# Performance work log

Measured on AMD Instinct MI355X. Metric: run time of the kernel, lower is better.

Reference implementation:

```python
import jax, jax.numpy as jnp
import numpy as np

EMBED = 1024
HEADS = 16
HEAD_DIM = EMBED // HEADS
HIDDEN = 4096
EPS = 1e-6


def _layer_norm(x, gamma, beta):
    mu = jnp.mean(x, axis=-1, keepdims=True)
    var = jnp.mean(jnp.square(x - mu), axis=-1, keepdims=True)
    return (x - mu) * jax.lax.rsqrt(var + EPS) * gamma + beta


def setup_inputs() -> dict:
    key = jax.random.key(0)
    ks = jax.random.split(key, 16)
    s = 1.0 / np.sqrt(EMBED)
    sh = 1.0 / np.sqrt(HIDDEN)
    return {
        "x": jax.random.normal(ks[0], (2, 2048, EMBED), dtype=jnp.float32),
        "Wq": jax.random.uniform(ks[1], (EMBED, EMBED), jnp.float32, -s, s),
        "bq": jnp.zeros((EMBED,), jnp.float32),
        "Wk": jax.random.uniform(ks[2], (EMBED, EMBED), jnp.float32, -s, s),
        "bk": jnp.zeros((EMBED,), jnp.float32),
        "Wv": jax.random.uniform(ks[3], (EMBED, EMBED), jnp.float32, -s, s),
        "bv": jnp.zeros((EMBED,), jnp.float32),
        "Wo": jax.random.uniform(ks[4], (EMBED, EMBED), jnp.float32, -s, s),
        "bo": jnp.zeros((EMBED,), jnp.float32),
        "ln1_g": jnp.ones((EMBED,), jnp.float32),
        "ln1_b": jnp.zeros((EMBED,), jnp.float32),
        "W1": jax.random.uniform(ks[5], (EMBED, HIDDEN), jnp.float32, -s, s),
        "b1": jnp.zeros((HIDDEN,), jnp.float32),
        "W2": jax.random.uniform(ks[6], (HIDDEN, EMBED), jnp.float32, -sh, sh),
        "b2": jnp.zeros((EMBED,), jnp.float32),
        "ln2_g": jnp.ones((EMBED,), jnp.float32),
        "ln2_b": jnp.zeros((EMBED,), jnp.float32),
    }


def reference(x, Wq, bq, Wk, bk, Wv, bv, Wo, bo, ln1_g, ln1_b, W1, b1, W2, b2, ln2_g, ln2_b):
    B, S, _ = x.shape
    # projections (weights stored as [in, out])
    q = (x @ Wq + bq).reshape(B, S, HEADS, HEAD_DIM)
    k = (x @ Wk + bk).reshape(B, S, HEADS, HEAD_DIM)
    v = (x @ Wv + bv).reshape(B, S, HEADS, HEAD_DIM)
    # scores: [B, H, S, S]
    scores = jnp.einsum('bqhd,bkhd->bhqk', q, k) / jnp.sqrt(jnp.float32(HEAD_DIM))
    attn = jax.nn.softmax(scores, axis=-1)
    ctx = jnp.einsum('bhqk,bkhd->bqhd', attn, v).reshape(B, S, EMBED)
    attn_out = ctx @ Wo + bo
    x1 = _layer_norm(x + attn_out, ln1_g, ln1_b)
    ffn = jax.nn.relu(x1 @ W1 + b1) @ W2 + b2
    return _layer_norm(x1 + ffn, ln2_g, ln2_b)
```

## Files before the change

kernel.cpp:

```cpp
#include <hip/hip_runtime.h>
#include <math.h>

#define EMBED 1024
#define HEADS 16
#define HDIM  64
#define HIDDEN 4096
#define BATCH 2
#define SEQ   2048
#define TOK   (BATCH * SEQ)

typedef _Float16 f16;
typedef f16 f16x8 __attribute__((ext_vector_type(8)));
typedef f16 f16x4 __attribute__((ext_vector_type(4)));
typedef float f32x4 __attribute__((ext_vector_type(4)));
typedef float f32x16 __attribute__((ext_vector_type(16)));

__device__ __forceinline__ void gload16(const void* g, void* s) {
  __builtin_amdgcn_global_load_lds(
      (const __attribute__((address_space(1))) unsigned int*)g,
      (__attribute__((address_space(3))) unsigned int*)s, 16, 0, 0);
}

template<int A16, int RELU, int OUT16, int QKV, int SPLITK>
__global__ __launch_bounds__(256, 3)
void gemm_f16(const void* __restrict__ Av, const f16* __restrict__ Wt,
              const float* __restrict__ bias0, const float* __restrict__ bias1,
              const float* __restrict__ bias2, void* __restrict__ Cv,
              int N, int K, int nbx) {
  __shared__ f16 As[512 * 8];
  __shared__ f16 Bs[512 * 8];
  const int tid = threadIdx.x;
  const int l = tid & 63, w = tid >> 6;
  const int g = l >> 4, ln = l & 15;
  int bid = blockIdx.x;
  int slice = 0;
  if (SPLITK > 1) { slice = bid % SPLITK; bid /= SPLITK; }
  const int ntiles = gridDim.x / SPLITK;
  const int cpx = ntiles >> 3;
  bid = (bid & 7) * cpx + (bid >> 3);
  const int m0 = (bid / nbx) << 7;
  const int n0 = (bid % nbx) << 7;
  const int wr = w >> 1, wc = w & 1;
  const int ksl = K / SPLITK;
  const int kbeg = slice * ksl, kend = kbeg + ksl;

  f32x4 acc[4][4] = {};

  for (int k0 = kbeg; k0 < kend; k0 += 32) {
    if (A16) {
      const f16* A = (const f16*)Av;
#pragma unroll
      for (int p = 0; p < 2; ++p) {
        const int u0 = p * 256 + w * 64;
        const int ks = u0 >> 7;
        const int row = ((u0 + l) & 127) ^ ks;
        gload16(A + (size_t)(m0 + row) * K + k0 + ks * 8, (void*)&As[u0 * 8]);
      }
    } else {
      const float* A = (const float*)Av;
      const int ks = tid & 3;
      const int r0 = tid >> 2;
#pragma unroll
      for (int p = 0; p < 2; ++p) {
        const int row = r0 + p * 64;
        const float* src = A + (size_t)(m0 + row) * K + k0 + ks * 8;
        float4 f0 = *(const float4*)src;
        float4 f1 = *(const float4*)(src + 4);
        f16x8 hh;
        hh[0] = (f16)f0.x; hh[1] = (f16)f0.y; hh[2] = (f16)f0.z; hh[3] = (f16)f0.w;
        hh[4] = (f16)f1.x; hh[5] = (f16)f1.y; hh[6] = (f16)f1.z; hh[7] = (f16)f1.w;
        *(f16x8*)&As[(ks * 128 + (row ^ ks)) * 8] = hh;
      }
    }
#pragma unroll
    for (int p = 0; p < 2; ++p) {
      const int u0 = p * 256 + w * 64;
      const int ks = u0 >> 7;
      const int col = ((u0 + l) & 127) ^ ks;
      gload16(Wt + (size_t)(n0 + col) * K + k0 + ks * 8, (void*)&Bs[u0 * 8]);
    }
    __syncthreads();
    f16x8 af[4], bf[4];
#pragma unroll
    for (int m = 0; m < 4; ++m)
      af[m] = *(const f16x8*)&As[(g * 128 + ((wr * 64 + m * 16 + ln) ^ g)) * 8];
#pragma unroll
    for (int n = 0; n < 4; ++n)
      bf[n] = *(const f16x8*)&Bs[(g * 128 + ((wc * 64 + n * 16 + ln) ^ g)) * 8];
#pragma unroll
    for (int m = 0; m < 4; ++m)
#pragma unroll
      for (int n = 0; n < 4; ++n)
        acc[m][n] = __builtin_amdgcn_mfma_f32_16x16x32_f16(af[m], bf[n], acc[m][n], 0, 0, 0);
    __syncthreads();
  }

  if (SPLITK > 1) {
    float* P = (float*)Cv + (size_t)slice * TOK * N;
#pragma unroll
    for (int m = 0; m < 4; ++m)
#pragma unroll
      for (int n = 0; n < 4; ++n)
#pragma unroll
        for (int r = 0; r < 4; ++r) {
          const size_t idx = (size_t)(m0 + wr * 64 + m * 16 + g * 4 + r) * N
                           + n0 + wc * 64 + n * 16 + ln;
          P[idx] = acc[m][n][r];
        }
    return;
  }

  const float* bp = bias0;
  int nbase = n0;
  float scale = 1.f;
  if (QKV) {
    const int seg = n0 >> 10;
    bp = (seg == 0) ? bias0 : (seg == 1) ? bias1 : bias2;
    nbase = n0 & 1023;
    if (seg == 0) scale = 0.125f * 1.44269504f;
  }
  float bv[4];
#pragma unroll
  for (int n = 0; n < 4; ++n) bv[n] = bp[nbase + wc * 64 + n * 16 + ln];
#pragma unroll
  for (int m = 0; m < 4; ++m)
#pragma unroll
    for (int n = 0; n < 4; ++n)
#pragma unroll
      for (int r = 0; r < 4; ++r) {
        float v = (acc[m][n][r] + bv[n]) * scale;
        if (RELU) v = fmaxf(v, 0.f);
        const size_t idx = (size_t)(m0 + wr * 64 + m * 16 + g * 4 + r) * N
                         + n0 + wc * 64 + n * 16 + ln;
        if (OUT16) ((f16*)Cv)[idx] = (f16)v;
        else       ((float*)Cv)[idx] = v;
      }
}

__device__ __forceinline__ unsigned kchunk(int key, int m) { return (unsigned)(m ^ (key & 7)); }

template<int BASE>
__device__ __forceinline__ f16x8 pack_frag(f32x16 p) {
  f16x8 r;
#pragma unroll
  for (int j = 0; j < 8; ++j) r[j] = (f16)p[BASE + j];
  return r;
}

#define VSTRIDE 68

__global__ __launch_bounds__(256, 2)
void attention(const f16* __restrict__ qkv, f16* __restrict__ ctx) {
  __shared__ f16 Ks[64 * 64];
  __shared__ f16 VT[64 * VSTRIDE];
  const int tid = threadIdx.x;
  const int l = tid & 63, w = tid >> 6;
  const int ln = l & 31, hi = l >> 5;
  const int bh = blockIdx.y, b = bh >> 4, h = bh & 15;
  const int q0 = blockIdx.x * 128;

  f16x8 qf[4];
  {
    const f16* qp = qkv + (size_t)(b * SEQ + q0 + w * 32 + ln) * 3072 + h * 64 + hi * 8;
#pragma unroll
    for (int kc = 0; kc < 4; ++kc) qf[kc] = *(const f16x8*)(qp + kc * 16);
  }

  f32x16 o0 = {}, o1 = {};
  float mrow = -1e30f, lrow = 0.f;

  const int skey = tid >> 3, sc = tid & 7;

  for (int kt = 0; kt < SEQ / 64; ++kt) {
    const size_t tb = (size_t)(b * SEQ + kt * 64) * 3072 + h * 64;
    f16x8 va = *(const f16x8*)(qkv + tb + 2048 + (size_t)skey * 3072 + sc * 8);
    f16x8 vb = *(const f16x8*)(qkv + tb + 2048 + (size_t)(32 + skey) * 3072 + sc * 8);
#pragma unroll
    for (int p = 0; p < 2; ++p) {
      const int key = p * 32 + skey;
      gload16(qkv + tb + 1024 + (size_t)key * 3072 + 8 * kchunk(key, sc),
              (void*)&Ks[(p * 256 + w * 64) * 8]);
    }
#pragma unroll
    for (int j = 0; j < 8; ++j) {
      const int d = sc * 8 + j;
      VT[d * VSTRIDE + skey] = va[j];
      VT[d * VSTRIDE + 32 + skey] = vb[j];
    }
    __syncthreads();

    f32x16 st0 = {}, st1 = {};
#pragma unroll
    for (int kc = 0; kc < 4; ++kc) {
      const int m = kc * 2 + hi;
      const f16x8 kf0 = *(const f16x8*)&Ks[(ln * 8 + (m ^ (ln & 7))) * 8];
      const f16x8 kf1 = *(const f16x8*)&Ks[((32 + ln) * 8 + (m ^ (ln & 7))) * 8];
      st0 = __builtin_amdgcn_mfma_f32_32x32x16_f16(kf0, qf[kc], st0, 0, 0, 0);
      st1 = __builtin_amdgcn_mfma_f32_32x32x16_f16(kf1, qf[kc], st1, 0, 0, 0);
    }

    float mt = st0[0];
#pragma unroll
    for (int r = 1; r < 16; ++r) mt = fmaxf(mt, st0[r]);
#pragma unroll
    for (int r = 0; r < 16; ++r) mt = fmaxf(mt, st1[r]);
    mt = fmaxf(mt, __shfl_xor(mt, 32));
    const float mn = fmaxf(mrow, mt);
    const float al = exp2f(mrow - mn);
    mrow = mn;
    float ps = 0.f;
#pragma unroll
    for (int r = 0; r < 16; ++r) { st0[r] = exp2f(st0[r] - mn); ps += st0[r]; }
#pragma unroll
    for (int r = 0; r < 16; ++r) { st1[r] = exp2f(st1[r] - mn); ps += st1[r]; }
    ps += __shfl_xor(ps, 32);
    lrow = lrow * al + ps;
#pragma unroll
    for (int r = 0; r < 16; ++r) { o0[r] *= al; o1[r] *= al; }

    f16x8 pf[4];
    pf[0] = pack_frag<0>(st0); pf[1] = pack_frag<8>(st0);
    pf[2] = pack_frag<0>(st1); pf[3] = pack_frag<8>(st1);

#pragma unroll
    for (int s = 0; s < 4; ++s) {
      const int k0a = 16 * s + 4 * hi;
      {
        const f16* p0 = &VT[ln * VSTRIDE + k0a];
        f16x4 x = *(const f16x4*)p0;
        f16x4 y = *(const f16x4*)(p0 + 8);
        f16x8 vf = __builtin_shufflevector(x, y, 0, 1, 2, 3, 4, 5, 6, 7);
        o0 = __builtin_amdgcn_mfma_f32_32x32x16_f16(vf, pf[s], o0, 0, 0, 0);
      }
      {
        const f16* p1 = &VT[(32 + ln) * VSTRIDE + k0a];
        f16x4 x = *(const f16x4*)p1;
        f16x4 y = *(const f16x4*)(p1 + 8);
        f16x8 vf = __builtin_shufflevector(x, y, 0, 1, 2, 3, 4, 5, 6, 7);
        o1 = __builtin_amdgcn_mfma_f32_32x32x16_f16(vf, pf[s], o1, 0, 0, 0);
      }
    }
    __syncthreads();
  }

  const float inv = 1.f / lrow;
  f16* cp = ctx + (size_t)(b * SEQ + q0 + w * 32 + ln) * EMBED + h * 64;
#pragma unroll
  for (int r = 0; r < 16; ++r) {
    const int drow = (r & 3) + 8 * (r >> 2) + 4 * hi;
    cp[drow] = (f16)(o0[r] * inv);
    cp[32 + drow] = (f16)(o1[r] * inv);
  }
}

template<int NP, int OUT16>
__global__ __launch_bounds__(256, 4)
void add_ln(const float* parts, const float* __restrict__ bias,
            const float* resid, const float* __restrict__ gam,
            const float* __restrict__ bet, float* out, f16* __restrict__ out16) {
  const int t = blockIdx.x;
  const int tid = threadIdx.x;
  const size_t base = (size_t)t * EMBED + tid * 4;
  float4 rv = *(const float4*)(resid + base);
  float4 bb = *(const float4*)(bias + tid * 4);
  float x0 = rv.x + bb.x, x1 = rv.y + bb.y, x2 = rv.z + bb.z, x3 = rv.w + bb.w;
#pragma unroll
  for (int p = 0; p < NP; ++p) {
    float4 pv = *(const float4*)(parts + (size_t)p * TOK * EMBED + base);
    x0 += pv.x; x1 += pv.y; x2 += pv.z; x3 += pv.w;
  }
  float s1 = x0 + x1 + x2 + x3;
  float s2 = x0 * x0 + x1 * x1 + x2 * x2 + x3 * x3;
  for (int off = 1; off < 64; off <<= 1) {
    s1 += __shfl_xor(s1, off);
    s2 += __shfl_xor(s2, off);
  }
  __shared__ float red[8];
  if ((tid & 63) == 0) { red[(tid >> 6) * 2] = s1; red[(tid >> 6) * 2 + 1] = s2; }
  __syncthreads();
  s1 = red[0] + red[2] + red[4] + red[6];
  s2 = red[1] + red[3] + red[5] + red[7];
  const float mu = s1 * (1.f / EMBED);
  const float var = s2 * (1.f / EMBED) - mu * mu;
  const float rstd = rsqrtf(var + 1e-6f);
  float4 gv = *(const float4*)(gam + tid * 4);
  float4 bv = *(const float4*)(bet + tid * 4);
  float4 ov;
  ov.x = (x0 - mu) * rstd * gv.x + bv.x;
  ov.y = (x1 - mu) * rstd * gv.y + bv.y;
  ov.z = (x2 - mu) * rstd * gv.z + bv.z;
  ov.w = (x3 - mu) * rstd * gv.w + bv.w;
  *(float4*)(out + base) = ov;
  if (OUT16) {
    f16x4 hh;
    hh[0] = (f16)ov.x; hh[1] = (f16)ov.y; hh[2] = (f16)ov.z; hh[3] = (f16)ov.w;
    *(f16x4*)(out16 + base) = hh;
  }
}

__device__ __forceinline__ void transpose_tile(const float* in, f16* out,
                                               int K, int N, int k0, int n0, int tid) {
  __shared__ float t[32][33];
  {
    const int ky = tid >> 3, nx = (tid & 7) * 4;
    float4 f = *(const float4*)(in + (size_t)(k0 + ky) * N + n0 + nx);
    t[ky][nx] = f.x; t[ky][nx + 1] = f.y; t[ky][nx + 2] = f.z; t[ky][nx + 3] = f.w;
  }
  __syncthreads();
  const int ny = tid >> 3, kx = (tid & 7) * 4;
  f16x4 hh;
  hh[0] = (f16)t[kx][ny];     hh[1] = (f16)t[kx + 1][ny];
  hh[2] = (f16)t[kx + 2][ny]; hh[3] = (f16)t[kx + 3][ny];
  *(f16x4*)(out + (size_t)(n0 + ny) * K + k0 + kx) = hh;
}

__global__ __launch_bounds__(256, 4)
void transpose_w(const float* __restrict__ in, f16* __restrict__ out,
                 int K, int N) {
  transpose_tile(in, out, K, N, blockIdx.y * 32, blockIdx.x * 32, threadIdx.x);
}

__global__ __launch_bounds__(256, 4)
void transpose_qkv(const float* __restrict__ w0, const float* __restrict__ w1,
                   const float* __restrict__ w2, f16* __restrict__ out) {
  const float* in = (blockIdx.z == 0) ? w0 : (blockIdx.z == 1) ? w1 : w2;
  f16* o = out + (size_t)blockIdx.z * 1024 * 1024;
  transpose_tile(in, o, 1024, 1024, blockIdx.y * 32, blockIdx.x * 32, threadIdx.x);
}

extern "C" void kernel_launch(void* const* d_in, const int* in_sizes, int n_in,
                              void* d_out, int out_size, void* d_ws, size_t ws_size,
                              hipStream_t stream) {
  const float* x    = (const float*)d_in[0];
  const float* Wq   = (const float*)d_in[1];
  const float* bq   = (const float*)d_in[2];
  const float* Wk   = (const float*)d_in[3];
  const float* bk   = (const float*)d_in[4];
  const float* Wv   = (const float*)d_in[5];
  const float* bv   = (const float*)d_in[6];
  const float* Wo   = (const float*)d_in[7];
  const float* bo   = (const float*)d_in[8];
  const float* ln1g = (const float*)d_in[9];
  const float* ln1b = (const float*)d_in[10];
  const float* W1   = (const float*)d_in[11];
  const float* b1   = (const float*)d_in[12];
  const float* W2   = (const float*)d_in[13];
  const float* b2   = (const float*)d_in[14];
  const float* ln2g = (const float*)d_in[15];
  const float* ln2b = (const float*)d_in[16];
  float* out = (float*)d_out;

  char* ws = (char*)d_ws;
  const size_t MB = 1024 * 1024;
  f16*   WtQKV = (f16*)(ws);
  f16*   WtO   = (f16*)(ws + 6 * MB);
  f16*   Wt1   = (f16*)(ws + 8 * MB);
  f16*   Wt2   = (f16*)(ws + 16 * MB);
  f16*   qkv   = (f16*)(ws + 24 * MB);
  f16*   ctx   = (f16*)(ws + 48 * MB);
  float* parts = (float*)(ws + 56 * MB);
  f16*   x1h   = (f16*)(ws + 88 * MB);
  f16*   hid   = (f16*)(ws + 24 * MB);
  float* x1    = out;

  const dim3 blk(256);
  transpose_qkv<<<dim3(32, 32, 3), blk, 0, stream>>>(Wq, Wk, Wv, WtQKV);
  transpose_w<<<dim3(32, 32), blk, 0, stream>>>(Wo, WtO, 1024, 1024);
  transpose_w<<<dim3(128, 32), blk, 0, stream>>>(W1, Wt1, 1024, 4096);
  transpose_w<<<dim3(32, 128), blk, 0, stream>>>(W2, Wt2, 4096, 1024);

  gemm_f16<0, 0, 1, 1, 1><<<768, blk, 0, stream>>>(x, WtQKV, bq, bk, bv, qkv, 3072, 1024, 24);
  attention<<<dim3(16, 32), blk, 0, stream>>>(qkv, ctx);
  gemm_f16<1, 0, 0, 0, 2><<<512, blk, 0, stream>>>(ctx, WtO, nullptr, nullptr, nullptr, parts, 1024, 1024, 8);
  add_ln<2, 1><<<4096, blk, 0, stream>>>(parts, bo, x, ln1g, ln1b, x1, x1h);
  gemm_f16<1, 1, 1, 0, 1><<<1024, blk, 0, stream>>>(x1h, Wt1, b1, nullptr, nullptr, hid, 4096, 1024, 32);
  gemm_f16<1, 0, 0, 0, 2><<<512, blk, 0, stream>>>(hid, Wt2, nullptr, nullptr, nullptr, parts, 1024, 4096, 8);
  add_ln<2, 0><<<4096, blk, 0, stream>>>(parts, b2, x1, ln2g, ln2b, out, nullptr);
}
```

Baseline: 451.7 us.

## Double-buffer K/V tiles in attention with lazy softmax rescale and swizzled V layout

The attention kernel now double-buffers the K and V^T tiles in shared memory, prefetching the next tile while computing the current one, so each iteration needs a single barrier. It adds a lazy online-softmax rescale that skips rescaling the O accumulators unless the row max grows by more than 8 (in log2 units), and tree reductions for the max and sum. It also XOR-swizzles the V^T shared layout to reduce bank conflicts and raises wave priority around the MFMA sections. The cost is double the shared-memory footprint, which may reduce occupancy, and the lazy rescale lets exponentials exceed 1 by a bounded factor, which stresses fp16 range in P.

```diff
diff --git a/kernel.cpp b/kernel.cpp
--- a/kernel.cpp
+++ b/kernel.cpp
@@ -137,8 +137,6 @@
       }
 }
 
-__device__ __forceinline__ unsigned kchunk(int key, int m) { return (unsigned)(m ^ (key & 7)); }
-
 template<int BASE>
 __device__ __forceinline__ f16x8 pack_frag(f32x16 p) {
   f16x8 r;
@@ -148,11 +146,12 @@
 }
 
 #define VSTRIDE 68
+#define NKT (SEQ / 64)
 
 __global__ __launch_bounds__(256, 2)
 void attention(const f16* __restrict__ qkv, f16* __restrict__ ctx) {
-  __shared__ f16 Ks[64 * 64];
-  __shared__ f16 VT[64 * VSTRIDE];
+  __shared__ f16 Ks[2][64 * 64];
+  __shared__ f16 VTs[2][64 * VSTRIDE];
   const int tid = threadIdx.x;
   const int l = tid & 63, w = tid >> 6;
   const int ln = l & 31, hi = l >> 5;
@@ -170,78 +169,120 @@
   float mrow = -1e30f, lrow = 0.f;
 
   const int skey = tid >> 3, sc = tid & 7;
-
-  for (int kt = 0; kt < SEQ / 64; ++kt) {
-    const size_t tb = (size_t)(b * SEQ + kt * 64) * 3072 + h * 64;
-    f16x8 va = *(const f16x8*)(qkv + tb + 2048 + (size_t)skey * 3072 + sc * 8);
-    f16x8 vb = *(const f16x8*)(qkv + tb + 2048 + (size_t)(32 + skey) * 3072 + sc * 8);
+  const f16* kbase = qkv + (size_t)(b * SEQ) * 3072 + 1024 + h * 64;
+  const f16* vbase = qkv + (size_t)(b * SEQ) * 3072 + 2048 + h * 64;
+  const int wbase = sc * 8 * VSTRIDE + (skey ^ (sc << 2));
+
+  auto gloadK = [&](int buf, int kt) {
 #pragma unroll
     for (int p = 0; p < 2; ++p) {
       const int key = p * 32 + skey;
-      gload16(qkv + tb + 1024 + (size_t)key * 3072 + 8 * kchunk(key, sc),
-              (void*)&Ks[(p * 256 + w * 64) * 8]);
-    }
+      gload16(kbase + (size_t)(kt * 64 + key) * 3072 + 8 * (sc ^ (key & 7)),
+              (void*)&Ks[buf][(p * 256 + w * 64) * 8]);
+    }
+  };
+  auto scatterV = [&](int buf, f16x8 va, f16x8 vb2) {
 #pragma unroll
     for (int j = 0; j < 8; ++j) {
-      const int d = sc * 8 + j;
-      VT[d * VSTRIDE + skey] = va[j];
-      VT[d * VSTRIDE + 32 + skey] = vb[j];
-    }
-    __syncthreads();
-
+      VTs[buf][wbase + VSTRIDE * j] = va[j];
+      VTs[buf][wbase + VSTRIDE * j + 32] = vb2[j];
+    }
+  };
+
+  {
+    const f16* vp = vbase + (size_t)skey * 3072 + sc * 8;
+    f16x8 va = *(const f16x8*)vp;
+    f16x8 vb2 = *(const f16x8*)(vp + (size_t)32 * 3072);
+    gloadK(0, 0);
+    scatterV(0, va, vb2);
+  }
+  __syncthreads();
+
+  const int sw0 = (ln >> 3) << 2;
+  const int db0 = ln * VSTRIDE, db1 = (32 + ln) * VSTRIDE;
+
+  auto body = [&](int kt, int cur) {
+    const int nxt = cur ^ 1;
+    f16x8 vna = {}, vnb = {};
+    const bool more = (kt + 1 < NKT);
+    if (more) {
+      const f16* vp = vbase + (size_t)((kt + 1) * 64 + skey) * 3072 + sc * 8;
+      vna = *(const f16x8*)vp;
+      vnb = *(const f16x8*)(vp + (size_t)32 * 3072);
+      gloadK(nxt, kt + 1);
+    }
     f32x16 st0 = {}, st1 = {};
+    __builtin_amdgcn_s_setprio(1);
 #pragma unroll
     for (int kc = 0; kc < 4; ++kc) {
       const int m = kc * 2 + hi;
-      const f16x8 kf0 = *(const f16x8*)&Ks[(ln * 8 + (m ^ (ln & 7))) * 8];
-      const f16x8 kf1 = *(const f16x8*)&Ks[((32 + ln) * 8 + (m ^ (ln & 7))) * 8];
+      const f16x8 kf0 = *(const f16x8*)&Ks[cur][(ln * 8 + (m ^ (ln & 7))) * 8];
+      const f16x8 kf1 = *(const f16x8*)&Ks[cur][((32 + ln) * 8 + (m ^ (ln & 7))) * 8];
       st0 = __builtin_amdgcn_mfma_f32_32x32x16_f16(kf0, qf[kc], st0, 0, 0, 0);
       st1 = __builtin_amdgcn_mfma_f32_32x32x16_f16(kf1, qf[kc], st1, 0, 0, 0);
     }
-
-    float mt = st0[0];
-#pragma unroll
-    for (int r = 1; r < 16; ++r) mt = fmaxf(mt, st0[r]);
-#pragma unroll
-    for (int r = 0; r < 16; ++r) mt = fmaxf(mt, st1[r]);
-    mt = fmaxf(mt, __shfl_xor(mt, 32));
-    const float mn = fmaxf(mrow, mt);
-    const float al = exp2f(mrow - mn);
-    mrow = mn;
-    float ps = 0.f;
-#pragma unroll
-    for (int r = 0; r < 16; ++r) { st0[r] = exp2f(st0[r] - mn); ps += st0[r]; }
-#pragma unroll
-    for (int r = 0; r < 16; ++r) { st1[r] = exp2f(st1[r] - mn); ps += st1[r]; }
-    ps += __shfl_xor(ps, 32);
-    lrow = lrow * al + ps;
-#pragma unroll
-    for (int r = 0; r < 16; ++r) { o0[r] *= al; o1[r] *= al; }
+    __builtin_amdgcn_s_setprio(0);
+
+    float tm[16];
+#pragma unroll
+    for (int r = 0; r < 16; ++r) tm[r] = fmaxf(st0[r], st1[r]);
+#pragma unroll
+    for (int s2 = 8; s2 >= 1; s2 >>= 1)
+#pragma unroll
+      for (int r = 0; r < s2; ++r) tm[r] = fmaxf(tm[r], tm[r + s2]);
+    const float mt = fmaxf(tm[0], __shfl_xor(tm[0], 32));
+    if (!__all(mt <= mrow + 8.f)) {
+      const float mn = fmaxf(mrow, mt);
+      const float al = exp2f(mrow - mn);
+      mrow = mn;
+      lrow *= al;
+#pragma unroll
+      for (int r = 0; r < 16; ++r) { o0[r] *= al; o1[r] *= al; }
+    }
+    float ts[16];
+#pragma unroll
+    for (int r = 0; r < 16; ++r) {
+      st0[r] = exp2f(st0[r] - mrow);
+      st1[r] = exp2f(st1[r] - mrow);
+      ts[r] = st0[r] + st1[r];
+    }
+#pragma unroll
+    for (int s2 = 8; s2 >= 1; s2 >>= 1)
+#pragma unroll
+      for (int r = 0; r < s2; ++r) ts[r] += ts[r + s2];
+    lrow += ts[0] + __shfl_xor(ts[0], 32);
 
     f16x8 pf[4];
     pf[0] = pack_frag<0>(st0); pf[1] = pack_frag<8>(st0);
     pf[2] = pack_frag<0>(st1); pf[3] = pack_frag<8>(st1);
 
+    __builtin_amdgcn_s_setprio(1);
 #pragma unroll
     for (int s = 0; s < 4; ++s) {
-      const int k0a = 16 * s + 4 * hi;
+      const int k0 = 16 * s + 4 * hi;
       {
-        const f16* p0 = &VT[ln * VSTRIDE + k0a];
-        f16x4 x = *(const f16x4*)p0;
-        f16x4 y = *(const f16x4*)(p0 + 8);
+        const int p0 = k0 ^ sw0;
+        f16x4 x = *(const f16x4*)&VTs[cur][db0 + p0];
+        f16x4 y = *(const f16x4*)&VTs[cur][db0 + (p0 ^ 8)];
         f16x8 vf = __builtin_shufflevector(x, y, 0, 1, 2, 3, 4, 5, 6, 7);
         o0 = __builtin_amdgcn_mfma_f32_32x32x16_f16(vf, pf[s], o0, 0, 0, 0);
       }
       {
-        const f16* p1 = &VT[(32 + ln) * VSTRIDE + k0a];
-        f16x4 x = *(const f16x4*)p1;
-        f16x4 y = *(const f16x4*)(p1 + 8);
+        const int p1 = k0 ^ sw0 ^ 16;
+        f16x4 x = *(const f16x4*)&VTs[cur][db1 + p1];
+        f16x4 y = *(const f16x4*)&VTs[cur][db1 + (p1 ^ 8)];
         f16x8 vf = __builtin_shufflevector(x, y, 0, 1, 2, 3, 4, 5, 6, 7);
         o1 = __builtin_amdgcn_mfma_f32_32x32x16_f16(vf, pf[s], o1, 0, 0, 0);
       }
     }
+    __builtin_amdgcn_s_setprio(0);
+
+    if (more) scatterV(nxt, vna, vnb);
     __syncthreads();
-  }
+  };
+
+#pragma unroll 1
+  for (int kt = 0; kt < NKT; kt += 2) { body(kt, 0); body(kt + 1, 1); }
 
   const float inv = 1.f / lrow;
   f16* cp = ctx + (size_t)(b * SEQ + q0 + w * 32 + ln) * EMBED + h * 64;
```

After: 448.1 us. No clear change (-0.8%).
